# Performance work log

Measured on AMD Instinct MI355X. Metric: run time of the kernel, lower is better.

The kernel has to match this reference:

```python
import jax, jax.numpy as jnp
import numpy as np

B, S, D, H = 8, 1024, 512, 12
HS = D // H  # 42 (head_size; 12*42 = 504 concat width, as in the original)


def setup_inputs() -> dict:
    key = jax.random.key(0)
    ks = jax.random.split(key, 12)
    sd = 0.02
    return {
        "embedded_patches": jax.random.normal(ks[0], (B, S, D), dtype=jnp.float32),
        # stacked per-head projections (12 independent Linear(D, HS, bias=False))
        "wk": jax.random.normal(ks[1], (H, D, HS), dtype=jnp.float32) * sd,
        "wq": jax.random.normal(ks[2], (H, D, HS), dtype=jnp.float32) * sd,
        "wv": jax.random.normal(ks[3], (H, D, HS), dtype=jnp.float32) * sd,
        "w_proj": jax.random.normal(ks[4], (H * HS, D), dtype=jnp.float32) * sd,  # [504, 512]
        "b_proj": jnp.zeros((D,), dtype=jnp.float32),
        # shared LayerNorm (same params used for both norms, as in the original)
        "gamma": jnp.ones((D,), dtype=jnp.float32),
        "beta": jnp.zeros((D,), dtype=jnp.float32),
        "w1": jax.random.normal(ks[5], (D, 4 * D), dtype=jnp.float32) * sd,
        "b1": jnp.zeros((4 * D,), dtype=jnp.float32),
        "w2": jax.random.normal(ks[6], (4 * D, D), dtype=jnp.float32) * sd,
        "b2": jnp.zeros((D,), dtype=jnp.float32),
    }


def _layernorm(x, gamma, beta, eps=1e-5):
    mu = jnp.mean(x, axis=-1, keepdims=True)
    var = jnp.var(x, axis=-1, keepdims=True)
    return (x - mu) * jax.lax.rsqrt(var + eps) * gamma + beta


def reference(embedded_patches, wk, wq, wv, w_proj, b_proj, gamma, beta, w1, b1, w2, b2):
    x = embedded_patches
    n1 = _layernorm(x, gamma, beta)
    # per-head projections, vectorized over heads: [B,S,D] x [H,D,E] -> [B,H,S,E]
    q = jnp.einsum('bsd,hde->bhse', n1, wq)
    k = jnp.einsum('bsd,hde->bhse', n1, wk)
    v = jnp.einsum('bsd,hde->bhse', n1, wv)
    scale = HS ** -0.5
    wei = jax.nn.softmax(jnp.einsum('bhse,bhte->bhst', q, k) * scale, axis=-1)
    out = jnp.einsum('bhst,bhte->bhse', wei, v)        # [B,H,S,E]
    out = out.transpose(0, 2, 1, 3).reshape(B, S, H * HS)  # concat heads -> [B,S,504]
    attn = out @ w_proj + b_proj                       # [B,S,D]
    # original quirk: takes batch element 0 and broadcasts against residual
    first_added = attn[0] + x                          # [S,D] + [B,S,D] -> [B,S,D]
    n2 = _layernorm(first_added, gamma, beta)
    h = jax.nn.gelu(n2 @ w1 + b1, approximate=False)   # torch nn.GELU default = exact erf
    ff = h @ w2 + b2
    return ff + first_added
```

## Files before the change

kernel.cpp:

```cpp
#include <hip/hip_runtime.h>
#include <hip/hip_bf16.h>
#include <stdint.h>


typedef unsigned short u16;
typedef __attribute__((ext_vector_type(8))) short short8;
typedef __attribute__((ext_vector_type(4))) float f32x4;

__device__ __forceinline__ u16 f2bf(float f) {
  union { float f; unsigned u; } x; x.f = f;
  return (u16)((x.u + 0x7FFFu + ((x.u >> 16) & 1u)) >> 16);
}
__device__ __forceinline__ float bf2f(u16 u) {
  union { unsigned u; float f; } x; x.u = ((unsigned)u) << 16;
  return x.f;
}

__device__ __forceinline__ void gload_lds16(const u16* g, u16* l) {
  __builtin_amdgcn_global_load_lds(
      (__attribute__((address_space(1))) void*)g,
      (__attribute__((address_space(3))) void*)l, 16, 0, 0);
}

__device__ __forceinline__ float wred_sum(float v) {
#pragma unroll
  for (int off = 32; off > 0; off >>= 1) v += __shfl_xor(v, off, 64);
  return v;
}

__device__ __forceinline__ float gelu_fast(float t) {
  const float p = __builtin_fmaf(0.0356774081f, t * t, 0.7978845608f);
  return t / (1.0f + __expf(-2.0f * t * p));
}

#define MFMA16x16(a, b, c) __builtin_amdgcn_mfma_f32_16x16x32_bf16(a, b, c, 0, 0, 0)

enum { EP_BF16 = 0, EP_F32B = 2, EP_GELU = 3, EP_ATOM = 7 };

template <int EP, int BK>
__device__ __forceinline__ void gemm_core(u16* lds, const u16* __restrict__ Ab,
                                          int lda, const u16* __restrict__ Bb,
                                          int ldb, void* __restrict__ Cv,
                                          int ldc, int K,
                                          const float* __restrict__ bias,
                                          int m0, int n0) {
  constexpr int GPR = BK / 8;
  constexpr int RPI = 64 / GPR;
  constexpr int IPM = 32 / RPI;
  constexpr int TSZ = 128 * BK;
  u16* lA[2] = {lds, lds + TSZ};
  u16* lB[2] = {lds + 2 * TSZ, lds + 3 * TSZ};

  const int tid = threadIdx.x;
  const int w = tid >> 6;
  const int l = tid & 63;
  const int wr = w >> 1;
  const int wc = w & 1;
  const int NT = K / BK;

  f32x4 acc[4][4];
#pragma unroll
  for (int i = 0; i < 4; ++i)
#pragma unroll
    for (int j = 0; j < 4; ++j) acc[i][j] = (f32x4){0.f, 0.f, 0.f, 0.f};

  const int srow = w * 32 + l / GPR;
  const int sk = (l % GPR) * 8;
  const u16* gA = Ab + (long)(m0 + srow) * lda + sk;
  const u16* gB = Bb + (long)(n0 + srow) * ldb + sk;
  const int dOff = w * 32 * BK;

  const int aoff = (wr * 64 + (l & 15)) * BK + (l >> 4) * 8;
  const int boff = (wc * 64 + (l & 15)) * BK + (l >> 4) * 8;

  auto stage = [&](int b_, int t_) {
#pragma unroll
    for (int i = 0; i < IPM; ++i) {
      gload_lds16(gA + (long)t_ * BK + (long)i * RPI * lda,
                  lA[b_] + dOff + i * RPI * BK);
      gload_lds16(gB + (long)t_ * BK + (long)i * RPI * ldb,
                  lB[b_] + dOff + i * RPI * BK);
    }
  };

  stage(0, 0);
  __syncthreads();

  int buf = 0;
  for (int t = 0; t < NT; ++t) {
    if (t + 1 < NT) stage(buf ^ 1, t + 1);
#pragma unroll
    for (int ks = 0; ks < BK / 32; ++ks) {
      short8 af[4], bfv[4];
#pragma unroll
      for (int mi = 0; mi < 4; ++mi)
        af[mi] = *(const short8*)&lA[buf][aoff + mi * 16 * BK + ks * 32];
#pragma unroll
      for (int ni = 0; ni < 4; ++ni)
        bfv[ni] = *(const short8*)&lB[buf][boff + ni * 16 * BK + ks * 32];
#pragma unroll
      for (int mi = 0; mi < 4; ++mi)
#pragma unroll
        for (int ni = 0; ni < 4; ++ni)
          acc[mi][ni] = MFMA16x16(af[mi], bfv[ni], acc[mi][ni]);
    }
    __syncthreads();
    buf ^= 1;
  }

  const int rbase = m0 + wr * 64 + (l >> 4) * 4;
  const int cbase = n0 + wc * 64 + (l & 15);
#pragma unroll
  for (int mi = 0; mi < 4; ++mi) {
#pragma unroll
    for (int ni = 0; ni < 4; ++ni) {
#pragma unroll
      for (int j = 0; j < 4; ++j) {
        const int row = rbase + mi * 16 + j;
        const int col = cbase + ni * 16;
        const float v = acc[mi][ni][j];
        if (EP == EP_BF16) {
          ((u16*)Cv)[(long)row * ldc + col] = f2bf(v);
        } else if (EP == EP_F32B) {
          ((float*)Cv)[(long)row * ldc + col] = v + bias[col];
        } else if (EP == EP_GELU) {
          ((u16*)Cv)[(long)row * ldc + col] = f2bf(gelu_fast(v + bias[col]));
        } else {
          atomicAdd(&((float*)Cv)[(long)row * ldc + col], v);
        }
      }
    }
  }
}

template <int EP, int BK>
__launch_bounds__(256, (BK == 32 ? 4 : 2))
__global__ void gemm_k(const u16* __restrict__ A, int lda, long sAz,
                       const u16* __restrict__ Bt, int ldb, long sBz,
                       void* __restrict__ Cv, int ldc, int K,
                       const float* __restrict__ bias) {
  __shared__ u16 lds[4 * 128 * BK];
  const int gx = gridDim.x, gy = gridDim.y, gz = gridDim.z;
  const int lin = blockIdx.x + gx * (blockIdx.y + gy * blockIdx.z);
  const int nwg = gx * gy * gz;
  const int wg = (lin & 7) * (nwg >> 3) + (lin >> 3);
  const int by = wg % gy;
  const int rem = wg / gy;
  const int z = rem % gz;
  const int bx = rem / gz;
  const u16* Ab = A + (long)z * sAz;
  const u16* Bb = Bt + (long)z * sBz;
  gemm_core<EP, BK>(lds, Ab, lda, Bb, ldb, Cv, ldc, K, bias, bx * 128,
                    by * 128);
}

__launch_bounds__(256, 4)
__global__ void qkvt_kernel(const u16* __restrict__ n1,
                            const u16* __restrict__ BtQKV,
                            u16* __restrict__ qkvc,
                            const u16* __restrict__ wvT,
                            u16* __restrict__ vt) {
  __shared__ u16 lds[4 * 128 * 32];
  const int lin = blockIdx.x;
  const int wg = (lin & 7) * 24 + (lin >> 3);
  if (wg < 96) {
    gemm_core<EP_BF16, 32>(lds, n1, 512, BtQKV, 512, qkvc, 1536, 512, nullptr,
                           (wg & 7) * 128, (wg >> 3) * 128);
  } else {
    const int v = wg - 96;
    gemm_core<EP_BF16, 32>(lds, wvT, 512, n1, 512, vt, 1024, 512, nullptr,
                           (v % 12) * 128, (v / 12) * 128);
  }
}

__device__ __forceinline__ short8 frag_read(const u16* base, int row, int ks,
                                            int l) {
  const int g = (ks * 4 + (l >> 4)) ^ (l & 7);
  return *(const short8*)&base[row * 64 + g * 8];
}

__launch_bounds__(256, 2)
__global__ void flash_attn(const u16* __restrict__ qkvc,
                           const u16* __restrict__ vt,
                           u16* __restrict__ cat) {
  __shared__ u16 lQ[64 * 64];
  __shared__ u16 lK[2][64 * 64];
  __shared__ u16 lV[2][64 * 64];
  __shared__ u16 lP[4][16 * 64];
  const int h = blockIdx.x;
  const int q0 = blockIdx.y * 64;
  const int tid = threadIdx.x;
  const int w = tid >> 6;
  const int l = tid & 63;
  const int sg = ((l & 7) ^ (l >> 3)) * 8;
  const int sr = w * 8 + (l >> 3);

#define FA_STAGE(t_, b_)                                                    \
  do {                                                                      \
    const int kv_ = (t_) * 64;                                              \
    gload_lds16(qkvc + (long)(kv_ + sr) * 1536 + 768 + h * 64 + sg,         \
                lK[b_] + w * 8 * 64);                                       \
    gload_lds16(qkvc + (long)(kv_ + 32 + sr) * 1536 + 768 + h * 64 + sg,    \
                lK[b_] + (32 + w * 8) * 64);                                \
    gload_lds16(vt + (long)(h * 128 + sr) * 1024 + kv_ + sg,                \
                lV[b_] + w * 8 * 64);                                       \
    gload_lds16(vt + (long)(h * 128 + 32 + sr) * 1024 + kv_ + sg,           \
                lV[b_] + (32 + w * 8) * 64);                                \
  } while (0)

  gload_lds16(qkvc + (long)(q0 + sr) * 1536 + h * 64 + sg, lQ + w * 8 * 64);
  gload_lds16(qkvc + (long)(q0 + 32 + sr) * 1536 + h * 64 + sg,
              lQ + (32 + w * 8) * 64);
  FA_STAGE(0, 0);
  __syncthreads();

  const short8 qf0 = frag_read(lQ, w * 16 + (l & 15), 0, l);
  const short8 qf1 = frag_read(lQ, w * 16 + (l & 15), 1, l);

  f32x4 accO[4];
  float m_run[4], l_run[4];
#pragma unroll
  for (int i = 0; i < 4; ++i) {
    accO[i] = (f32x4){0.f, 0.f, 0.f, 0.f};
    m_run[i] = -3.0e38f;
    l_run[i] = 0.f;
  }

  int buf = 0;
  for (int t = 0; t < 16; ++t) {
    if (t + 1 < 16) FA_STAGE(t + 1, buf ^ 1);
    f32x4 s[4];
#pragma unroll
    for (int ni = 0; ni < 4; ++ni) {
      const short8 kf0 = frag_read(lK[buf], ni * 16 + (l & 15), 0, l);
      const short8 kf1 = frag_read(lK[buf], ni * 16 + (l & 15), 1, l);
      s[ni] = MFMA16x16(qf0, kf0, ((f32x4){0.f, 0.f, 0.f, 0.f}));
      s[ni] = MFMA16x16(qf1, kf1, s[ni]);
    }
#pragma unroll
    for (int j = 0; j < 4; ++j) {
      float mx = fmaxf(fmaxf(s[0][j], s[1][j]), fmaxf(s[2][j], s[3][j]));
      mx = fmaxf(mx, __shfl_xor(mx, 1));
      mx = fmaxf(mx, __shfl_xor(mx, 2));
      mx = fmaxf(mx, __shfl_xor(mx, 4));
      mx = fmaxf(mx, __shfl_xor(mx, 8));
      const float mn = fmaxf(m_run[j], mx);
      const float corr = __expf(m_run[j] - mn);
      m_run[j] = mn;
      float ps = 0.f;
#pragma unroll
      for (int ni = 0; ni < 4; ++ni) {
        const float p = __expf(s[ni][j] - mn);
        s[ni][j] = p;
        ps += p;
      }
      ps += __shfl_xor(ps, 1);
      ps += __shfl_xor(ps, 2);
      ps += __shfl_xor(ps, 4);
      ps += __shfl_xor(ps, 8);
      l_run[j] = l_run[j] * corr + ps;
#pragma unroll
      for (int ne = 0; ne < 4; ++ne) accO[ne][j] *= corr;
    }
#pragma unroll
    for (int ni = 0; ni < 4; ++ni) {
#pragma unroll
      for (int j = 0; j < 4; ++j) {
        const int row = (l >> 4) * 4 + j;
        const int col = ni * 16 + (l & 15);
        const int boff = row * 128 + (((col >> 3) ^ (row & 7)) << 4) +
                         (col & 7) * 2;
        *(u16*)((char*)lP[w] + boff) = f2bf(s[ni][j]);
      }
    }
    asm volatile("s_waitcnt lgkmcnt(0)" ::: "memory");
    __builtin_amdgcn_sched_barrier(0);
    const short8 pf0 = frag_read(lP[w], (l & 15), 0, l);
    const short8 pf1 = frag_read(lP[w], (l & 15), 1, l);
#pragma unroll
    for (int ne = 0; ne < 4; ++ne) {
      const short8 vf0 = frag_read(lV[buf], ne * 16 + (l & 15), 0, l);
      const short8 vf1 = frag_read(lV[buf], ne * 16 + (l & 15), 1, l);
      accO[ne] = MFMA16x16(pf0, vf0, accO[ne]);
      accO[ne] = MFMA16x16(pf1, vf1, accO[ne]);
    }
    __syncthreads();
    buf ^= 1;
  }
#undef FA_STAGE

#pragma unroll
  for (int j = 0; j < 4; ++j) {
    const float inv = 1.0f / l_run[j];
    const int row = q0 + w * 16 + (l >> 4) * 4 + j;
#pragma unroll
    for (int ne = 0; ne < 4; ++ne) {
      const int e = ne * 16 + (l & 15);
      if (e < 42)
        cat[(long)row * 512 + h * 42 + e] = f2bf(accO[ne][j] * inv);
    }
  }
}

__device__ __forceinline__ void transpose_body(const float* __restrict__ in,
                                               u16* __restrict__ out, int N,
                                               int Kin, int Kpad, int blk,
                                               int gx, int t, float* smem) {
  const int n0 = (blk % gx) * 64;
  const int k0 = (blk / gx) * 64;
  const int tc = t & 63;
  const int tr = t >> 6;
#pragma unroll
  for (int r = 0; r < 16; ++r) {
    const int kr = tr * 16 + r;
    const int kg = k0 + kr;
    smem[kr * 65 + tc] = (kg < Kin) ? in[(long)kg * N + n0 + tc] : 0.f;
  }
  __syncthreads();
  const int nr0 = t >> 4;
  const int kc = (t & 15) * 4;
#pragma unroll
  for (int p = 0; p < 4; ++p) {
    const int nr = nr0 + p * 16;
    ushort4 v;
    v.x = f2bf(smem[(kc + 0) * 65 + nr]);
    v.y = f2bf(smem[(kc + 1) * 65 + nr]);
    v.z = f2bf(smem[(kc + 2) * 65 + nr]);
    v.w = f2bf(smem[(kc + 3) * 65 + nr]);
    *(ushort4*)&out[(long)(n0 + nr) * Kpad + k0 + kc] = v;
  }
}

__global__ void prep_fused(const float* __restrict__ wq,
                           const float* __restrict__ wk,
                           const float* __restrict__ wv,
                           const float* __restrict__ w_proj,
                           const float* __restrict__ w1,
                           const float* __restrict__ w2,
                           const float* __restrict__ x,
                           const float* __restrict__ gamma,
                           const float* __restrict__ beta,
                           u16* __restrict__ BtQKV, u16* __restrict__ wvT,
                           u16* __restrict__ BtP, u16* __restrict__ Bt1,
                           u16* __restrict__ Bt2, u16* __restrict__ cat,
                           u16* __restrict__ n1, float scale) {
  __shared__ float smem[64 * 65];
  const int blk = blockIdx.x;
  const int t = threadIdx.x;
  if (blk < 3072) {
    const int i = blk * 256 + t;
    const int n = i >> 9, d = i & 511;
    const int pq = n / 768;
    const int h = (n % 768) >> 6;
    const int e = n & 63;
    float v = 0.f;
    if (e < 42) {
      v = (pq ? wk : wq)[((long)h * 512 + d) * 42 + e];
      if (!pq) v *= scale;
    }
    BtQKV[i] = f2bf(v);
  } else if (blk < 6144) {
    const int i = (blk - 3072) * 256 + t;
    const int r = i >> 9, d = i & 511;
    const int h = r >> 7, e = r & 127;
    wvT[i] = f2bf(e < 42 ? wv[((long)h * 512 + d) * 42 + e] : 0.f);
  } else if (blk < 6208) {
    transpose_body(w_proj, BtP, 512, 504, 512, blk - 6144, 8, t, smem);
  } else if (blk < 6464) {
    transpose_body(w1, Bt1, 2048, 512, 512, blk - 6208, 32, t, smem);
  } else if (blk < 6720) {
    transpose_body(w2, Bt2, 512, 2048, 2048, blk - 6464, 8, t, smem);
  } else if (blk < 8768) {
    cat[(blk - 6720) * 256 + t] = 0;
  } else {
    const int s = blk - 8768;
    const float* row = x + (long)s * 512;
    const float v0 = row[t];
    const float v1 = row[t + 256];
    float sum = wred_sum(v0 + v1);
    float sq = wred_sum(v0 * v0 + v1 * v1);
    if ((t & 63) == 0) { smem[t >> 6] = sum; smem[8 + (t >> 6)] = sq; }
    __syncthreads();
    sum = smem[0] + smem[1] + smem[2] + smem[3];
    sq = smem[8] + smem[9] + smem[10] + smem[11];
    const float mu = sum * (1.0f / 512.0f);
    const float rstd = rsqrtf(sq * (1.0f / 512.0f) - mu * mu + 1e-5f);
    n1[(long)s * 512 + t] = f2bf((v0 - mu) * rstd * gamma[t] + beta[t]);
    n1[(long)s * 512 + t + 256] =
        f2bf((v1 - mu) * rstd * gamma[t + 256] + beta[t + 256]);
  }
}

__global__ void ln2_kernel(const float* __restrict__ x,
                           const float* __restrict__ aproj,
                           const float* __restrict__ gamma,
                           const float* __restrict__ beta,
                           const float* __restrict__ b2,
                           u16* __restrict__ n2, float* __restrict__ outp) {
  __shared__ float red[16];
  const int r = blockIdx.x;
  const int t = threadIdx.x;
  const int s = r & 1023;
  const float* xr = x + (long)r * 512;
  const float* ar = aproj + (long)s * 512;
  const float v0 = xr[t] + ar[t];
  const float v1 = xr[t + 256] + ar[t + 256];
  outp[(long)r * 512 + t] = v0 + b2[t];
  outp[(long)r * 512 + t + 256] = v1 + b2[t + 256];
  float sum = wred_sum(v0 + v1);
  float sq = wred_sum(v0 * v0 + v1 * v1);
  if ((t & 63) == 0) { red[t >> 6] = sum; red[8 + (t >> 6)] = sq; }
  __syncthreads();
  sum = red[0] + red[1] + red[2] + red[3];
  sq = red[8] + red[9] + red[10] + red[11];
  const float mu = sum * (1.0f / 512.0f);
  const float rstd = rsqrtf(sq * (1.0f / 512.0f) - mu * mu + 1e-5f);
  n2[(long)r * 512 + t] = f2bf((v0 - mu) * rstd * gamma[t] + beta[t]);
  n2[(long)r * 512 + t + 256] =
      f2bf((v1 - mu) * rstd * gamma[t + 256] + beta[t + 256]);
}

extern "C" void kernel_launch(void* const* d_in, const int* in_sizes, int n_in,
                              void* d_out, int out_size, void* d_ws,
                              size_t ws_size, hipStream_t stream) {
  const float* x = (const float*)d_in[0];
  const float* wk = (const float*)d_in[1];
  const float* wq = (const float*)d_in[2];
  const float* wv = (const float*)d_in[3];
  const float* w_proj = (const float*)d_in[4];
  const float* b_proj = (const float*)d_in[5];
  const float* gamma = (const float*)d_in[6];
  const float* beta = (const float*)d_in[7];
  const float* w1 = (const float*)d_in[8];
  const float* b1 = (const float*)d_in[9];
  const float* w2 = (const float*)d_in[10];
  const float* b2 = (const float*)d_in[11];

  char* base = (char*)d_ws;
  size_t off = 0;
  auto alloc = [&](size_t bytes) -> void* {
    void* p = base + off;
    off += (bytes + 255) & ~(size_t)255;
    return p;
  };
  u16* n1 = (u16*)alloc(1024L * 512 * 2);
  u16* qkvc = (u16*)alloc(1024L * 1536 * 2);
  u16* wvT = (u16*)alloc(1536L * 512 * 2);
  u16* vt = (u16*)alloc(1536L * 1024 * 2);
  u16* cat = (u16*)alloc(1024L * 512 * 2);
  float* aproj = (float*)alloc(1024L * 512 * 4);
  u16* n2 = (u16*)alloc(8192L * 512 * 2);
  u16* hbuf = (u16*)alloc(8192L * 2048 * 2);
  u16* BtQKV = (u16*)alloc(1536L * 512 * 2);
  u16* BtP = (u16*)alloc(512L * 512 * 2);
  u16* Bt1 = (u16*)alloc(2048L * 512 * 2);
  u16* Bt2 = (u16*)alloc(512L * 2048 * 2);
  (void)ws_size; (void)in_sizes; (void)n_in; (void)out_size;

  const float scale = 0.15430334996209191f;

  prep_fused<<<9792, 256, 0, stream>>>(wq, wk, wv, w_proj, w1, w2, x, gamma,
                                       beta, BtQKV, wvT, BtP, Bt1, Bt2, cat,
                                       n1, scale);
  qkvt_kernel<<<192, 256, 0, stream>>>(n1, BtQKV, qkvc, wvT, vt);
  flash_attn<<<dim3(12, 16), 256, 0, stream>>>(qkvc, vt, cat);
  gemm_k<EP_F32B, 32><<<dim3(8, 4, 1), 256, 0, stream>>>(
      cat, 512, 0, BtP, 512, 0, aproj, 512, 512, b_proj);
  ln2_kernel<<<8192, 256, 0, stream>>>(x, aproj, gamma, beta, b2, n2,
                                       (float*)d_out);
  gemm_k<EP_GELU, 32><<<dim3(64, 16, 1), 256, 0, stream>>>(
      n2, 512, 0, Bt1, 512, 0, hbuf, 2048, 512, b1);
  gemm_k<EP_ATOM, 64><<<dim3(64, 4, 2), 256, 0, stream>>>(
      hbuf, 2048, 1024, Bt2, 2048, 1024, d_out, 512, 1024, nullptr);
}
```

Measured before the change: 158.1 us.

## Use 256x128 eight-wave GEMM tiles for FFN and hoist LDS fragment reads

```diff
diff --git a/kernel.cpp b/kernel.cpp
--- a/kernel.cpp
+++ b/kernel.cpp
@@ -37,26 +37,23 @@
 
 enum { EP_BF16 = 0, EP_F32B = 2, EP_GELU = 3, EP_ATOM = 7 };
 
-template <int EP, int BK>
+template <int EP, int TM>
 __device__ __forceinline__ void gemm_core(u16* lds, const u16* __restrict__ Ab,
                                           int lda, const u16* __restrict__ Bb,
                                           int ldb, void* __restrict__ Cv,
                                           int ldc, int K,
                                           const float* __restrict__ bias,
                                           int m0, int n0) {
-  constexpr int GPR = BK / 8;
-  constexpr int RPI = 64 / GPR;
-  constexpr int IPM = 32 / RPI;
-  constexpr int TSZ = 128 * BK;
-  u16* lA[2] = {lds, lds + TSZ};
-  u16* lB[2] = {lds + 2 * TSZ, lds + 3 * TSZ};
+  constexpr int ASZ = TM * 32;
+  u16* lA[2] = {lds, lds + ASZ};
+  u16* lB[2] = {lds + 2 * ASZ, lds + 2 * ASZ + 4096};
 
   const int tid = threadIdx.x;
   const int w = tid >> 6;
   const int l = tid & 63;
   const int wr = w >> 1;
   const int wc = w & 1;
-  const int NT = K / BK;
+  const int NT = K >> 5;
 
   f32x4 acc[4][4];
 #pragma unroll
@@ -64,23 +61,22 @@
 #pragma unroll
     for (int j = 0; j < 4; ++j) acc[i][j] = (f32x4){0.f, 0.f, 0.f, 0.f};
 
-  const int srow = w * 32 + l / GPR;
-  const int sk = (l % GPR) * 8;
-  const u16* gA = Ab + (long)(m0 + srow) * lda + sk;
-  const u16* gB = Bb + (long)(n0 + srow) * ldb + sk;
-  const int dOff = w * 32 * BK;
-
-  const int aoff = (wr * 64 + (l & 15)) * BK + (l >> 4) * 8;
-  const int boff = (wc * 64 + (l & 15)) * BK + (l >> 4) * 8;
+  const int sk = (l & 3) * 8;
+  const u16* gA = Ab + (long)(m0 + w * 32 + (l >> 2)) * lda + sk;
+  const int dOffA = w * 1024;
+  const int srowB = (TM == 128) ? (w * 32 + (l >> 2)) : (w * 16 + (l >> 2));
+  const u16* gB = Bb + (long)(n0 + srowB) * ldb + sk;
+  const int dOffB = (TM == 128) ? w * 1024 : w * 512;
+
+  const int aoff = (wr * 64 + (l & 15)) * 32 + (l >> 4) * 8;
+  const int boff = (wc * 64 + (l & 15)) * 32 + (l >> 4) * 8;
 
   auto stage = [&](int b_, int t_) {
-#pragma unroll
-    for (int i = 0; i < IPM; ++i) {
-      gload_lds16(gA + (long)t_ * BK + (long)i * RPI * lda,
-                  lA[b_] + dOff + i * RPI * BK);
-      gload_lds16(gB + (long)t_ * BK + (long)i * RPI * ldb,
-                  lB[b_] + dOff + i * RPI * BK);
-    }
+    const int k0 = t_ * 32;
+    gload_lds16(gA + k0, lA[b_] + dOffA);
+    gload_lds16(gA + k0 + 16 * lda, lA[b_] + dOffA + 512);
+    gload_lds16(gB + k0, lB[b_] + dOffB);
+    if (TM == 128) gload_lds16(gB + k0 + 16 * ldb, lB[b_] + dOffB + 512);
   };
 
   stage(0, 0);
@@ -88,22 +84,19 @@
 
   int buf = 0;
   for (int t = 0; t < NT; ++t) {
+    short8 af[4], bfv[4];
+#pragma unroll
+    for (int mi = 0; mi < 4; ++mi)
+      af[mi] = *(const short8*)&lA[buf][aoff + mi * 16 * 32];
+#pragma unroll
+    for (int ni = 0; ni < 4; ++ni)
+      bfv[ni] = *(const short8*)&lB[buf][boff + ni * 16 * 32];
     if (t + 1 < NT) stage(buf ^ 1, t + 1);
 #pragma unroll
-    for (int ks = 0; ks < BK / 32; ++ks) {
-      short8 af[4], bfv[4];
-#pragma unroll
-      for (int mi = 0; mi < 4; ++mi)
-        af[mi] = *(const short8*)&lA[buf][aoff + mi * 16 * BK + ks * 32];
+    for (int mi = 0; mi < 4; ++mi)
 #pragma unroll
       for (int ni = 0; ni < 4; ++ni)
-        bfv[ni] = *(const short8*)&lB[buf][boff + ni * 16 * BK + ks * 32];
-#pragma unroll
-      for (int mi = 0; mi < 4; ++mi)
-#pragma unroll
-        for (int ni = 0; ni < 4; ++ni)
-          acc[mi][ni] = MFMA16x16(af[mi], bfv[ni], acc[mi][ni]);
-    }
+        acc[mi][ni] = MFMA16x16(af[mi], bfv[ni], acc[mi][ni]);
     __syncthreads();
     buf ^= 1;
   }
@@ -133,13 +126,13 @@
   }
 }
 
-template <int EP, int BK>
-__launch_bounds__(256, (BK == 32 ? 4 : 2))
+template <int EP, int TM>
+__launch_bounds__(TM * 2, 2)
 __global__ void gemm_k(const u16* __restrict__ A, int lda, long sAz,
                        const u16* __restrict__ Bt, int ldb, long sBz,
                        void* __restrict__ Cv, int ldc, int K,
                        const float* __restrict__ bias) {
-  __shared__ u16 lds[4 * 128 * BK];
+  __shared__ u16 lds[2 * TM * 32 + 2 * 128 * 32];
   const int gx = gridDim.x, gy = gridDim.y, gz = gridDim.z;
   const int lin = blockIdx.x + gx * (blockIdx.y + gy * blockIdx.z);
   const int nwg = gx * gy * gz;
@@ -150,7 +143,7 @@
   const int bx = rem / gz;
   const u16* Ab = A + (long)z * sAz;
   const u16* Bb = Bt + (long)z * sBz;
-  gemm_core<EP, BK>(lds, Ab, lda, Bb, ldb, Cv, ldc, K, bias, bx * 128,
+  gemm_core<EP, TM>(lds, Ab, lda, Bb, ldb, Cv, ldc, K, bias, bx * TM,
                     by * 128);
 }
 
@@ -164,12 +157,12 @@
   const int lin = blockIdx.x;
   const int wg = (lin & 7) * 24 + (lin >> 3);
   if (wg < 96) {
-    gemm_core<EP_BF16, 32>(lds, n1, 512, BtQKV, 512, qkvc, 1536, 512, nullptr,
-                           (wg & 7) * 128, (wg >> 3) * 128);
+    gemm_core<EP_BF16, 128>(lds, n1, 512, BtQKV, 512, qkvc, 1536, 512,
+                            nullptr, (wg & 7) * 128, (wg >> 3) * 128);
   } else {
     const int v = wg - 96;
-    gemm_core<EP_BF16, 32>(lds, wvT, 512, n1, 512, vt, 1024, 512, nullptr,
-                           (v % 12) * 128, (v / 12) * 128);
+    gemm_core<EP_BF16, 128>(lds, wvT, 512, n1, 512, vt, 1024, 512, nullptr,
+                            (v % 12) * 128, (v / 12) * 128);
   }
 }
 
@@ -464,12 +457,12 @@
                                        n1, scale);
   qkvt_kernel<<<192, 256, 0, stream>>>(n1, BtQKV, qkvc, wvT, vt);
   flash_attn<<<dim3(12, 16), 256, 0, stream>>>(qkvc, vt, cat);
-  gemm_k<EP_F32B, 32><<<dim3(8, 4, 1), 256, 0, stream>>>(
+  gemm_k<EP_F32B, 128><<<dim3(8, 4, 1), 256, 0, stream>>>(
       cat, 512, 0, BtP, 512, 0, aproj, 512, 512, b_proj);
   ln2_kernel<<<8192, 256, 0, stream>>>(x, aproj, gamma, beta, b2, n2,
                                        (float*)d_out);
-  gemm_k<EP_GELU, 32><<<dim3(64, 16, 1), 256, 0, stream>>>(
+  gemm_k<EP_GELU, 256><<<dim3(32, 16, 1), 512, 0, stream>>>(
       n2, 512, 0, Bt1, 512, 0, hbuf, 2048, 512, b1);
-  gemm_k<EP_ATOM, 64><<<dim3(64, 4, 2), 256, 0, stream>>>(
+  gemm_k<EP_ATOM, 256><<<dim3(32, 4, 2), 512, 0, stream>>>(
       hbuf, 2048, 1024, Bt2, 2048, 1024, d_out, 512, 1024, nullptr);
 }
```

New measurement: 173.0 us. 9.4% more time.
